# Performance work log

Measured on AMD Instinct MI355X. Metric: run time of the kernel, lower is better.

Reference implementation:

```python
import jax, jax.numpy as jnp
import numpy as np

N_NODES = 100000
N_EDGES = 1600000
N_GRAPHS = 64
FEAT = 64
EMB = 64
HID = 64
VOCAB = 32


def setup_inputs() -> dict:
    key = jax.random.key(0)
    ks = jax.random.split(key, 20)
    w = lambda k, sh: (jax.random.normal(k, sh, jnp.float32) * 0.05)
    x = jax.random.normal(ks[0], (N_NODES, FEAT), jnp.float32)
    edge_index = jax.random.randint(ks[1], (2, N_EDGES), 0, N_NODES, dtype=jnp.int32).astype(jnp.int64)
    batch = jnp.sort(jax.random.randint(ks[2], (N_NODES,), 0, N_GRAPHS, dtype=jnp.int32)).astype(jnp.int64)
    return {
        'x': x, 'edge_index': edge_index, 'batch': batch,
        # RGCN layer 1 (single relation): relation weight, root weight, bias
        'W1': w(ks[3], (FEAT, EMB)), 'root1': w(ks[4], (FEAT, EMB)), 'b1': w(ks[5], (EMB,)),
        # RGCN layer 2
        'W2': w(ks[6], (EMB, HID)), 'root2': w(ks[7], (EMB, HID)), 'b2': w(ks[8], (HID,)),
        # init_h / init_c linear heads
        'Wh': w(ks[9], (HID, HID)), 'bh': w(ks[10], (HID,)),
        'Wc': w(ks[11], (HID, HID)), 'bc': w(ks[12], (HID,)),
        # output layer
        'Wo': w(ks[13], (HID, VOCAB)), 'bo': w(ks[14], (VOCAB,)),
    }


def _rgcn(x, edge_index, W, root, b):
    # PyG RGCNConv with num_relations=1, aggr='mean':
    # out[i] = mean_{j in N(i)} (x[j] @ W) + x[i] @ root + b
    src, dst = edge_index[0], edge_index[1]
    msg = x[src] @ W                                    # [E, out] gather + small GEMM
    agg = jax.ops.segment_sum(msg, dst, num_segments=x.shape[0])
    cnt = jax.ops.segment_sum(jnp.ones((edge_index.shape[1],), x.dtype), dst, num_segments=x.shape[0])
    agg = agg / jnp.maximum(cnt, 1.0)[:, None]
    return agg + x @ root + b


def reference(x, edge_index, batch, W1, root1, b1, W2, root2, b2, Wh, bh, Wc, bc, Wo, bo):
    h = jax.nn.relu(_rgcn(x, edge_index, W1, root1, b1))
    h = jax.nn.relu(_rgcn(h, edge_index, W2, root2, b2))
    # global_mean_pool over graph-assignment vector `batch`
    summ = jax.ops.segment_sum(h, batch, num_segments=N_GRAPHS)
    cnt = jax.ops.segment_sum(jnp.ones((h.shape[0],), h.dtype), batch, num_segments=N_GRAPHS)
    pooled = summ / jnp.maximum(cnt, 1.0)[:, None]      # [G, HID]
    hidden = pooled @ Wh + bh
    cell = pooled @ Wc + bc
    logits = jax.nn.log_softmax(hidden @ Wo + bo, axis=1)
    return (logits, hidden, cell)
```

## Files before the change

### kernel.cpp

```cpp
#include <hip/hip_runtime.h>
#include <hip/hip_bf16.h>


typedef __attribute__((ext_vector_type(8))) short short8;
typedef __attribute__((ext_vector_type(4))) float f32x4;
typedef __attribute__((ext_vector_type(2))) float f32x2;

#define RB 9
#define MAXBINS 256
#define CAP 12288
#define BCAP 14336
#define CHUNK 8192

__device__ inline float bf2f(unsigned short h) {
    return __uint_as_float(((unsigned int)h) << 16);
}
__device__ inline float bflo(unsigned int u) { return __uint_as_float(u << 16); }
__device__ inline float bfhi(unsigned int u) { return __uint_as_float(u & 0xffff0000u); }
__device__ inline unsigned short f2bf(float f) {
    unsigned int u = __float_as_uint(f);
    u = (u + 0x7fffu + ((u >> 16) & 1u)) >> 16;
    return (unsigned short)u;
}

__device__ inline void build_bfrag(const float* __restrict__ W,
                                   const float* __restrict__ R,
                                   int q, int mm, short8 bfrag[8][2]) {
#pragma unroll
    for (int t = 0; t < 8; ++t) {
        const int n = t * 16 + mm;
        const float* P = (n < 64) ? (W + n) : (R + n - 64);
#pragma unroll
        for (int c = 0; c < 2; ++c) {
#pragma unroll
            for (int j = 0; j < 8; ++j) {
                const int k = c * 32 + q * 8 + j;
                bfrag[t][c][j] = (short)f2bf(P[k * 64]);
            }
        }
    }
}

__device__ inline void store_xw_fp8(unsigned char* __restrict__ xw8, int rowbase, int q,
                                    int t, int mm, const f32x4& accT, int N) {
#pragma unroll
    for (int r = 0; r < 4; ++r) {
        const float v0 = accT[r];
        const float v1 = __shfl_down(v0, 1);
        const float v2 = __shfl_down(v0, 2);
        const float v3 = __shfl_down(v0, 3);
        const int orow = rowbase + q * 4 + r;
        if (!(mm & 3) && orow < N) {
            unsigned int u = (unsigned int)__builtin_amdgcn_cvt_pk_fp8_f32(v0, v1, 0, false);
            u = (unsigned int)__builtin_amdgcn_cvt_pk_fp8_f32(v2, v3, (int)u, true);
            *(unsigned int*)&xw8[(size_t)orow * 64 + t * 16 + mm] = u;
        }
    }
}

__global__ __launch_bounds__(256) void bin_gemm1(const int* __restrict__ src,
                                                 const int* __restrict__ dst,
                                                 unsigned int* __restrict__ coarse,
                                                 int* __restrict__ gcur,
                                                 int E, int BINS, int nbBin,
                                                 const float* __restrict__ x,
                                                 const float* __restrict__ W1,
                                                 const float* __restrict__ R1,
                                                 const float* __restrict__ bias,
                                                 unsigned char* __restrict__ xw8,
                                                 unsigned short* __restrict__ xrb,
                                                 int N) {
    __shared__ int cnt[MAXBINS];
    __shared__ int incl[MAXBINS];
    __shared__ int bstart[MAXBINS];
    __shared__ int bcur[MAXBINS];
    __shared__ int gbase[MAXBINS];
    __shared__ unsigned int stage[CHUNK];
    __shared__ unsigned char binOf[CHUNK];

    const int tid = threadIdx.x;
    if (blockIdx.x >= (unsigned)nbBin) {
        const int gb = blockIdx.x - nbBin;
        if (gb == 0 && tid < 16)
            *(unsigned int*)&xw8[(size_t)N * 64 + tid * 4] = 0u;

        const int lane = tid & 63;
        const int q = lane >> 4;
        const int mm = lane & 15;

        short8 bfrag[8][2];
        build_bfrag(W1, R1, q, mm, bfrag);
        float bv[4];
#pragma unroll
        for (int tt = 0; tt < 4; ++tt) bv[tt] = bias[tt * 16 + mm];

        const int wid = tid >> 6;
        const int gw = gb * 4 + wid;
        const int nw = 1024 * 4;
        const int ntiles = N >> 4;

        for (int tile = gw; tile < ntiles; tile += nw) {
            const int row0 = tile << 4;
            const float* ap = &x[(size_t)(row0 + mm) * 64 + q * 8];
            const float4 f0 = *(const float4*)ap;
            const float4 f1 = *(const float4*)(ap + 4);
            const float4 f2 = *(const float4*)(ap + 32);
            const float4 f3 = *(const float4*)(ap + 36);
            short8 a0, a1;
            a0[0] = (short)f2bf(f0.x); a0[1] = (short)f2bf(f0.y);
            a0[2] = (short)f2bf(f0.z); a0[3] = (short)f2bf(f0.w);
            a0[4] = (short)f2bf(f1.x); a0[5] = (short)f2bf(f1.y);
            a0[6] = (short)f2bf(f1.z); a0[7] = (short)f2bf(f1.w);
            a1[0] = (short)f2bf(f2.x); a1[1] = (short)f2bf(f2.y);
            a1[2] = (short)f2bf(f2.z); a1[3] = (short)f2bf(f2.w);
            a1[4] = (short)f2bf(f3.x); a1[5] = (short)f2bf(f3.y);
            a1[6] = (short)f2bf(f3.z); a1[7] = (short)f2bf(f3.w);
            f32x4 acc[8];
#pragma unroll
            for (int t = 0; t < 8; ++t) {
                acc[t] = (f32x4){0.f, 0.f, 0.f, 0.f};
                acc[t] = __builtin_amdgcn_mfma_f32_16x16x32_bf16(a0, bfrag[t][0], acc[t], 0, 0, 0);
                acc[t] = __builtin_amdgcn_mfma_f32_16x16x32_bf16(a1, bfrag[t][1], acc[t], 0, 0, 0);
            }
#pragma unroll
            for (int t = 0; t < 4; ++t) store_xw_fp8(xw8, row0, q, t, mm, acc[t], N);
#pragma unroll
            for (int t = 4; t < 8; ++t) {
#pragma unroll
                for (int r = 0; r < 4; ++r) {
                    const float v = acc[t][r] + bv[t - 4];
                    const float vn = __shfl_down(v, 1);
                    if (!(mm & 1)) {
                        const unsigned int u = (unsigned int)f2bf(v) | ((unsigned int)f2bf(vn) << 16);
                        *(unsigned int*)&xrb[(size_t)(row0 + q * 4 + r) * 64 + (t - 4) * 16 + mm] = u;
                    }
                }
            }
        }
        return;
    }

    const int chunk0 = blockIdx.x * CHUNK;
    int myS[32], myD[32];
#pragma unroll
    for (int k = 0; k < 32; ++k) {
        const int idx = chunk0 + k * 256 + tid;
        if (idx < E) { myS[k] = src[idx]; myD[k] = dst[idx]; }
        else myD[k] = -1;
    }
    cnt[tid] = 0;
    __syncthreads();
#pragma unroll
    for (int k = 0; k < 32; ++k)
        if (myD[k] >= 0) atomicAdd(&cnt[myD[k] >> RB], 1);
    __syncthreads();
    incl[tid] = cnt[tid];
    __syncthreads();
    for (int off = 1; off < 256; off <<= 1) {
        int t = (tid >= off) ? incl[tid - off] : 0;
        __syncthreads();
        incl[tid] += t;
        __syncthreads();
    }
    bstart[tid] = incl[tid] - cnt[tid];
    bcur[tid] = incl[tid] - cnt[tid];
    __syncthreads();
#pragma unroll
    for (int k = 0; k < 32; ++k) {
        if (myD[k] >= 0) {
            const int b = myD[k] >> RB;
            const int pos = atomicAdd(&bcur[b], 1);
            stage[pos] = (unsigned int)myS[k] | ((unsigned int)(myD[k] & ((1 << RB) - 1)) << 17);
            binOf[pos] = (unsigned char)b;
        }
    }
    __syncthreads();
    if (tid < BINS && cnt[tid] > 0)
        gbase[tid] = tid * CAP + atomicAdd(&gcur[tid], cnt[tid]);
    __syncthreads();
    int total = E - chunk0;
    if (total > CHUNK) total = CHUNK;
    for (int idx = tid; idx < total; idx += 256) {
        const int b = binOf[idx];
        coarse[gbase[b] + (idx - bstart[b])] = stage[idx];
    }
}

__global__ __launch_bounds__(256) void finalize_csr(const unsigned int* __restrict__ coarse,
                                                    const int* __restrict__ gcur,
                                                    int* __restrict__ bucket,
                                                    int* __restrict__ pstart,
                                                    int* __restrict__ degarr,
                                                    int N, int BINS) {
    __shared__ int ncnt[512];
    __shared__ int pexcl[512];
    __shared__ int ncur[512];
    __shared__ int s2[256];

    const int tid = threadIdx.x;
    const int b = blockIdx.x;
    const int cb = gcur[b];
    const int base = b * BCAP;
    const unsigned int* reg = coarse + (size_t)b * CAP;
    const int node0 = b << RB;
    int nloc = N - node0;
    if (nloc > 512) nloc = 512;

    ncnt[tid] = 0; ncnt[tid + 256] = 0;
    __syncthreads();
    for (int idx = tid; idx < cb; idx += 256)
        atomicAdd(&ncnt[reg[idx] >> 17], 1);
    __syncthreads();
    const int p0 = (ncnt[2 * tid] + 15) & ~15;
    const int p1 = (ncnt[2 * tid + 1] + 15) & ~15;
    s2[tid] = p0 + p1;
    __syncthreads();
    for (int off = 1; off < 256; off <<= 1) {
        int t = (tid >= off) ? s2[tid - off] : 0;
        __syncthreads();
        s2[tid] += t;
        __syncthreads();
    }
    const int pairExcl = s2[tid] - (p0 + p1);
    pexcl[2 * tid] = pairExcl;
    pexcl[2 * tid + 1] = pairExcl + p0;
    ncur[2 * tid] = pairExcl;
    ncur[2 * tid + 1] = pairExcl + p0;
    __syncthreads();
    for (int i = tid; i < nloc; i += 256) {
        pstart[node0 + i] = base + pexcl[i];
        degarr[node0 + i] = ncnt[i];
        const int dg = ncnt[i];
        const int pd = (dg + 15) & ~15;
        for (int j = dg; j < pd; ++j) bucket[base + pexcl[i] + j] = N;
    }
    for (int idx = tid; idx < cb; idx += 256) {
        const unsigned int e = reg[idx];
        const int p = atomicAdd(&ncur[e >> 17], 1);
        bucket[base + p] = (int)(e & 0x1FFFFu);
    }
}

__global__ __launch_bounds__(256) void aggregate(const unsigned char* __restrict__ xw8,
                                                 const unsigned short* __restrict__ xrb,
                                                 const int* __restrict__ pstart,
                                                 const int* __restrict__ degarr,
                                                 const int* __restrict__ bucket,
                                                 unsigned short* __restrict__ outb,
                                                 int N) {
    const int lane = threadIdx.x & 63;
    const int quarter = lane >> 4;
    const int fl = lane & 15;
    const int wid = threadIdx.x >> 6;
    const int gw = blockIdx.x * 4 + wid;
    const int nw = gridDim.x * 4;

    for (int i = gw; i < N; i += 2 * nw) {
        const int iA = i;
        const int iB = i + nw;
        const bool hasB = iB < N;
        const int r0A = pstart[iA];
        const int dgA = degarr[iA];
        int r0B = r0A, dgB = 0;
        if (hasB) { r0B = pstart[iB]; dgB = degarr[iB]; }
        const int pdA = (dgA + 15) & ~15;
        const int pdB = (dgB + 15) & ~15;
        const int pdM = pdA > pdB ? pdA : pdB;

        float aA0 = 0.f, aA1 = 0.f, aA2 = 0.f, aA3 = 0.f;
        float aB0 = 0.f, aB1 = 0.f, aB2 = 0.f, aB3 = 0.f;
        for (int base = 0; base < pdM; base += 64) {
            const int remA = pdA - base;
            const int remB = pdB - base;
            const int sA = (lane < remA) ? bucket[r0A + base + lane] : N;
            const int sB = (lane < remB) ? bucket[r0B + base + lane] : N;
            int mx = pdM - base;
            if (mx > 64) mx = 64;
            for (int t = 0; t < mx; t += 16) {
                unsigned int uA[4], uB[4];
#pragma unroll
                for (int p = 0; p < 4; ++p) {
                    const int rrA = __shfl(sA, t + 4 * p + quarter);
                    uA[p] = *(const unsigned int*)&xw8[(size_t)rrA * 64 + fl * 4];
                }
#pragma unroll
                for (int p = 0; p < 4; ++p) {
                    const int rrB = __shfl(sB, t + 4 * p + quarter);
                    uB[p] = *(const unsigned int*)&xw8[(size_t)rrB * 64 + fl * 4];
                }
#pragma unroll
                for (int p = 0; p < 4; ++p) {
                    const f32x2 lo = __builtin_amdgcn_cvt_pk_f32_fp8(uA[p], false);
                    const f32x2 hi = __builtin_amdgcn_cvt_pk_f32_fp8(uA[p], true);
                    aA0 += lo.x; aA1 += lo.y; aA2 += hi.x; aA3 += hi.y;
                }
#pragma unroll
                for (int p = 0; p < 4; ++p) {
                    const f32x2 lo = __builtin_amdgcn_cvt_pk_f32_fp8(uB[p], false);
                    const f32x2 hi = __builtin_amdgcn_cvt_pk_f32_fp8(uB[p], true);
                    aB0 += lo.x; aB1 += lo.y; aB2 += hi.x; aB3 += hi.y;
                }
            }
        }
        aA0 += __shfl_xor(aA0, 16); aA1 += __shfl_xor(aA1, 16);
        aA2 += __shfl_xor(aA2, 16); aA3 += __shfl_xor(aA3, 16);
        aA0 += __shfl_xor(aA0, 32); aA1 += __shfl_xor(aA1, 32);
        aA2 += __shfl_xor(aA2, 32); aA3 += __shfl_xor(aA3, 32);
        aB0 += __shfl_xor(aB0, 16); aB1 += __shfl_xor(aB1, 16);
        aB2 += __shfl_xor(aB2, 16); aB3 += __shfl_xor(aB3, 16);
        aB0 += __shfl_xor(aB0, 32); aB1 += __shfl_xor(aB1, 32);
        aB2 += __shfl_xor(aB2, 32); aB3 += __shfl_xor(aB3, 32);

        if (quarter == 0) {
            const float invA = 1.0f / (float)(dgA > 0 ? dgA : 1);
            const uint2 urA = *(const uint2*)&xrb[(size_t)iA * 64 + fl * 4];
            const float o0 = fmaxf(aA0 * invA + bflo(urA.x), 0.f);
            const float o1 = fmaxf(aA1 * invA + bfhi(urA.x), 0.f);
            const float o2 = fmaxf(aA2 * invA + bflo(urA.y), 0.f);
            const float o3 = fmaxf(aA3 * invA + bfhi(urA.y), 0.f);
            uint2 w;
            w.x = (unsigned int)f2bf(o0) | ((unsigned int)f2bf(o1) << 16);
            w.y = (unsigned int)f2bf(o2) | ((unsigned int)f2bf(o3) << 16);
            *(uint2*)&outb[(size_t)iA * 64 + fl * 4] = w;
            if (hasB) {
                const float invB = 1.0f / (float)(dgB > 0 ? dgB : 1);
                const uint2 urB = *(const uint2*)&xrb[(size_t)iB * 64 + fl * 4];
                const float p0 = fmaxf(aB0 * invB + bflo(urB.x), 0.f);
                const float p1 = fmaxf(aB1 * invB + bfhi(urB.x), 0.f);
                const float p2 = fmaxf(aB2 * invB + bflo(urB.y), 0.f);
                const float p3 = fmaxf(aB3 * invB + bfhi(urB.y), 0.f);
                uint2 w2;
                w2.x = (unsigned int)f2bf(p0) | ((unsigned int)f2bf(p1) << 16);
                w2.y = (unsigned int)f2bf(p2) | ((unsigned int)f2bf(p3) << 16);
                *(uint2*)&outb[(size_t)iB * 64 + fl * 4] = w2;
            }
        }
    }
}

__global__ __launch_bounds__(256) void gemm_xwr2(const unsigned short* __restrict__ xin,
                                                 const float* __restrict__ W2,
                                                 const float* __restrict__ R2,
                                                 const float* __restrict__ bias,
                                                 unsigned char* __restrict__ xw8,
                                                 unsigned short* __restrict__ xrb,
                                                 int M) {
    if (blockIdx.x == 0 && threadIdx.x < 16)
        *(unsigned int*)&xw8[(size_t)M * 64 + threadIdx.x * 4] = 0u;

    const int lane = threadIdx.x & 63;
    const int q = lane >> 4;
    const int mm = lane & 15;

    short8 bfrag[8][2];
    build_bfrag(W2, R2, q, mm, bfrag);
    float bv[4];
#pragma unroll
    for (int tt = 0; tt < 4; ++tt) bv[tt] = bias[tt * 16 + mm];

    const int wid = threadIdx.x >> 6;
    const int gw = blockIdx.x * 4 + wid;
    const int nw = gridDim.x * 4;
    const int ntiles = M >> 4;

    for (int tile = gw; tile < ntiles; tile += nw) {
        const int row0 = tile << 4;
        const short8 a0 = *(const short8*)&xin[(size_t)(row0 + mm) * 64 + q * 8];
        const short8 a1 = *(const short8*)&xin[(size_t)(row0 + mm) * 64 + 32 + q * 8];
        f32x4 acc[8];
#pragma unroll
        for (int t = 0; t < 8; ++t) {
            acc[t] = (f32x4){0.f, 0.f, 0.f, 0.f};
            acc[t] = __builtin_amdgcn_mfma_f32_16x16x32_bf16(a0, bfrag[t][0], acc[t], 0, 0, 0);
            acc[t] = __builtin_amdgcn_mfma_f32_16x16x32_bf16(a1, bfrag[t][1], acc[t], 0, 0, 0);
        }
#pragma unroll
        for (int t = 0; t < 4; ++t) store_xw_fp8(xw8, row0, q, t, mm, acc[t], M);
#pragma unroll
        for (int t = 4; t < 8; ++t) {
#pragma unroll
            for (int r = 0; r < 4; ++r) {
                const float v = acc[t][r] + bv[t - 4];
                const float vn = __shfl_down(v, 1);
                if (!(mm & 1)) {
                    const unsigned int u = (unsigned int)f2bf(v) | ((unsigned int)f2bf(vn) << 16);
                    *(unsigned int*)&xrb[(size_t)(row0 + q * 4 + r) * 64 + (t - 4) * 16 + mm] = u;
                }
            }
        }
    }
}

__global__ __launch_bounds__(256) void pool_kernel(const unsigned short* __restrict__ h,
                                                   const int* __restrict__ batch,
                                                   float* __restrict__ pooled, int N) {
    __shared__ float red[16][64];
    __shared__ int bnds[2];
    const int gph = blockIdx.x;
    if (threadIdx.x < 2) {
        const int target = gph + threadIdx.x;
        int lo = 0, hi = N;
        while (lo < hi) {
            int mid = (lo + hi) >> 1;
            if (batch[mid] < target) lo = mid + 1; else hi = mid;
        }
        bnds[threadIdx.x] = lo;
    }
    __syncthreads();
    const int r0 = bnds[0], r1 = bnds[1];
    const int f = threadIdx.x & 15;
    const int r = threadIdx.x >> 4;
    float4 acc = {0.f, 0.f, 0.f, 0.f};
    for (int row = r0 + r; row < r1; row += 16) {
        const ushort4 v = *(const ushort4*)&h[(size_t)row * 64 + f * 4];
        acc.x += bf2f(v.x); acc.y += bf2f(v.y);
        acc.z += bf2f(v.z); acc.w += bf2f(v.w);
    }
    red[r][f * 4 + 0] = acc.x; red[r][f * 4 + 1] = acc.y;
    red[r][f * 4 + 2] = acc.z; red[r][f * 4 + 3] = acc.w;
    __syncthreads();
    if (threadIdx.x < 64) {
        float s = 0.f;
        for (int j = 0; j < 16; ++j) s += red[j][threadIdx.x];
        const int cnt = r1 - r0;
        const float invc = 1.0f / (float)(cnt > 0 ? cnt : 1);
        pooled[gph * 64 + threadIdx.x] = s * invc;
    }
}

__global__ __launch_bounds__(256) void head_kernel(const float* __restrict__ pooled,
                                                   const float* __restrict__ Wh,
                                                   const float* __restrict__ bh,
                                                   const float* __restrict__ Wc,
                                                   const float* __restrict__ bc,
                                                   const float* __restrict__ Wo,
                                                   const float* __restrict__ bo,
                                                   float* __restrict__ out) {
    __shared__ float pm[4096];
    __shared__ float Ws[4096];
    __shared__ float Cs[4096];
    __shared__ float hid[4096];
    const int t = threadIdx.x;

    for (int idx = t; idx < 1024; idx += 256) {
        ((float4*)pm)[idx] = ((const float4*)pooled)[idx];
        ((float4*)Ws)[idx] = ((const float4*)Wh)[idx];
        ((float4*)Cs)[idx] = ((const float4*)Wc)[idx];
    }
    __syncthreads();

    const int w = t >> 6;
    const int l = t & 63;
    const float bhv = bh[l], bcv = bc[l];
    float ah[16], ac[16];
#pragma unroll
    for (int i = 0; i < 16; ++i) { ah[i] = bhv; ac[i] = bcv; }
    const float* pmw = pm + ((w << 4) << 6);
#pragma unroll 4
    for (int k = 0; k < 64; ++k) {
        const float wv = Ws[(k << 6) + l];
        const float cv = Cs[(k << 6) + l];
#pragma unroll
        for (int i = 0; i < 16; ++i) {
            const float p = pmw[(i << 6) + k];
            ah[i] = fmaf(p, wv, ah[i]);
            ac[i] = fmaf(p, cv, ac[i]);
        }
    }
#pragma unroll
    for (int i = 0; i < 16; ++i) {
        const int g = (w << 4) + i;
        hid[(g << 6) + l] = ah[i];
        out[2048 + (g << 6) + l] = ah[i];
        out[6144 + (g << 6) + l] = ac[i];
    }
    __syncthreads();
    for (int idx = t; idx < 512; idx += 256)
        ((float4*)Ws)[idx] = ((const float4*)Wo)[idx];
    __syncthreads();

    const int v = l & 31;
    const int gh = l >> 5;
    const int g0 = ((w << 1) + gh) << 3;
    const float bov = bo[v];
    float lgacc[8];
#pragma unroll
    for (int i = 0; i < 8; ++i) lgacc[i] = bov;
#pragma unroll 4
    for (int k = 0; k < 64; ++k) {
        const float wv = Ws[(k << 5) + v];
#pragma unroll
        for (int i = 0; i < 8; ++i)
            lgacc[i] = fmaf(hid[((g0 + i) << 6) + k], wv, lgacc[i]);
    }
    float* lg = pm;
#pragma unroll
    for (int i = 0; i < 8; ++i) lg[((g0 + i) << 5) + v] = lgacc[i];
    __syncthreads();

    const int g = t >> 2;
    const int vs = (t & 3) << 3;
    const float* row = lg + (g << 5);
    float mx = -3.4e38f;
#pragma unroll
    for (int j = 0; j < 8; ++j) mx = fmaxf(mx, row[vs + j]);
    mx = fmaxf(mx, __shfl_xor(mx, 1));
    mx = fmaxf(mx, __shfl_xor(mx, 2));
    float s = 0.f;
#pragma unroll
    for (int j = 0; j < 8; ++j) s += __expf(row[vs + j] - mx);
    s += __shfl_xor(s, 1);
    s += __shfl_xor(s, 2);
    const float lse = mx + __logf(s);
#pragma unroll
    for (int j = 0; j < 8; ++j) out[(g << 5) + vs + j] = row[vs + j] - lse;
}

extern "C" void kernel_launch(void* const* d_in, const int* in_sizes, int n_in,
                              void* d_out, int out_size, void* d_ws, size_t ws_size,
                              hipStream_t stream) {
    const float* x = (const float*)d_in[0];
    const int* ei = (const int*)d_in[1];
    const int* batch = (const int*)d_in[2];
    const float* W1 = (const float*)d_in[3];
    const float* root1 = (const float*)d_in[4];
    const float* b1 = (const float*)d_in[5];
    const float* W2 = (const float*)d_in[6];
    const float* root2 = (const float*)d_in[7];
    const float* b2 = (const float*)d_in[8];
    const float* Wh = (const float*)d_in[9];
    const float* bh = (const float*)d_in[10];
    const float* Wc = (const float*)d_in[11];
    const float* bc = (const float*)d_in[12];
    const float* Wo = (const float*)d_in[13];
    const float* bo = (const float*)d_in[14];
    float* out = (float*)d_out;

    const int N = in_sizes[0] / 64;
    const int E = in_sizes[1] / 2;
    const int* srcp = ei;
    const int* dstp = ei + E;
    const int BINS = (N + (1 << RB) - 1) >> RB;

    char* ws = (char*)d_ws;
    size_t off = 0;
    auto alloc = [&](size_t bytes) -> void* {
        void* p = ws + off;
        off += (bytes + 255) & ~(size_t)255;
        return p;
    };
    int* pstart = (int*)alloc((size_t)N * 4);
    int* degarr = (int*)alloc((size_t)N * 4);
    int* bucket = (int*)alloc(((size_t)BINS * BCAP + 256) * 4);
    unsigned int* coarse = (unsigned int*)alloc((size_t)BINS * CAP * 4);
    unsigned short* h1 = (unsigned short*)alloc((size_t)N * 64 * 2);
    unsigned short* h2 = (unsigned short*)alloc((size_t)N * 64 * 2);
    unsigned char* xw8 = (unsigned char*)alloc((size_t)(N + 1) * 64);
    unsigned char* xw8b = (unsigned char*)alloc((size_t)(N + 1) * 64);
    unsigned short* xrb = (unsigned short*)alloc((size_t)N * 64 * 2);
    unsigned short* xrb2 = (unsigned short*)alloc((size_t)N * 64 * 2);
    float* pooled = (float*)alloc(4096 * 4);
    int* gcur = (int*)alloc(MAXBINS * 4);

    const int nbBin = (E + CHUNK - 1) / CHUNK;

    hipMemsetAsync(gcur, 0, MAXBINS * 4, stream);
    bin_gemm1<<<nbBin + 1024, 256, 0, stream>>>(srcp, dstp, coarse, gcur, E, BINS, nbBin,
                                                x, W1, root1, b1, xw8, xrb, N);
    finalize_csr<<<BINS, 256, 0, stream>>>(coarse, gcur, bucket, pstart, degarr, N, BINS);
    aggregate<<<4096, 256, 0, stream>>>(xw8, xrb, pstart, degarr, bucket, h1, N);
    gemm_xwr2<<<1024, 256, 0, stream>>>(h1, W2, root2, b2, xw8b, xrb2, N);
    aggregate<<<4096, 256, 0, stream>>>(xw8b, xrb2, pstart, degarr, bucket, h2, N);
    pool_kernel<<<64, 256, 0, stream>>>(h2, batch, pooled, N);
    head_kernel<<<1, 256, 0, stream>>>(pooled, Wh, bh, Wc, bc, Wo, bo, out);
}
```

Baseline: 263.8 us.

## Split pooling across four blocks per graph and skip padded gather work in aggregate

```diff
diff --git a/kernel.cpp b/kernel.cpp
--- a/kernel.cpp
+++ b/kernel.cpp
@@ -254,6 +254,7 @@
     const int wid = threadIdx.x >> 6;
     const int gw = blockIdx.x * 4 + wid;
     const int nw = gridDim.x * 4;
+    const unsigned flo = (unsigned)(fl << 2);
 
     for (int i = gw; i < N; i += 2 * nw) {
         const int iA = i;
@@ -272,33 +273,48 @@
         for (int base = 0; base < pdM; base += 64) {
             const int remA = pdA - base;
             const int remB = pdB - base;
-            const int sA = (lane < remA) ? bucket[r0A + base + lane] : N;
-            const int sB = (lane < remB) ? bucket[r0B + base + lane] : N;
+            int sA = N, sB = N;
+            if (remA > 0 && lane < remA)
+                sA = *(const int*)((const char*)bucket + ((unsigned)(r0A + base + lane) << 2));
+            if (remB > 0 && lane < remB)
+                sB = *(const int*)((const char*)bucket + ((unsigned)(r0B + base + lane) << 2));
+            const int mxA = remA < 64 ? remA : 64;
+            const int mxB = remB < 64 ? remB : 64;
             int mx = pdM - base;
             if (mx > 64) mx = 64;
             for (int t = 0; t < mx; t += 16) {
+                const bool doA = t < mxA;
+                const bool doB = t < mxB;
                 unsigned int uA[4], uB[4];
-#pragma unroll
-                for (int p = 0; p < 4; ++p) {
-                    const int rrA = __shfl(sA, t + 4 * p + quarter);
-                    uA[p] = *(const unsigned int*)&xw8[(size_t)rrA * 64 + fl * 4];
+                if (doA) {
+#pragma unroll
+                    for (int p = 0; p < 4; ++p) {
+                        const unsigned rr = (unsigned)__shfl(sA, t + 4 * p + quarter);
+                        uA[p] = *(const unsigned int*)(xw8 + ((rr << 6) | flo));
+                    }
                 }
-#pragma unroll
-                for (int p = 0; p < 4; ++p) {
-                    const int rrB = __shfl(sB, t + 4 * p + quarter);
-                    uB[p] = *(const unsigned int*)&xw8[(size_t)rrB * 64 + fl * 4];
+                if (doB) {
+#pragma unroll
+                    for (int p = 0; p < 4; ++p) {
+                        const unsigned rr = (unsigned)__shfl(sB, t + 4 * p + quarter);
+                        uB[p] = *(const unsigned int*)(xw8 + ((rr << 6) | flo));
+                    }
                 }
-#pragma unroll
-                for (int p = 0; p < 4; ++p) {
-                    const f32x2 lo = __builtin_amdgcn_cvt_pk_f32_fp8(uA[p], false);
-                    const f32x2 hi = __builtin_amdgcn_cvt_pk_f32_fp8(uA[p], true);
-                    aA0 += lo.x; aA1 += lo.y; aA2 += hi.x; aA3 += hi.y;
+                if (doA) {
+#pragma unroll
+                    for (int p = 0; p < 4; ++p) {
+                        const f32x2 lo = __builtin_amdgcn_cvt_pk_f32_fp8(uA[p], false);
+                        const f32x2 hi = __builtin_amdgcn_cvt_pk_f32_fp8(uA[p], true);
+                        aA0 += lo.x; aA1 += lo.y; aA2 += hi.x; aA3 += hi.y;
+                    }
                 }
-#pragma unroll
-                for (int p = 0; p < 4; ++p) {
-                    const f32x2 lo = __builtin_amdgcn_cvt_pk_f32_fp8(uB[p], false);
-                    const f32x2 hi = __builtin_amdgcn_cvt_pk_f32_fp8(uB[p], true);
-                    aB0 += lo.x; aB1 += lo.y; aB2 += hi.x; aB3 += hi.y;
+                if (doB) {
+#pragma unroll
+                    for (int p = 0; p < 4; ++p) {
+                        const f32x2 lo = __builtin_amdgcn_cvt_pk_f32_fp8(uB[p], false);
+                        const f32x2 hi = __builtin_amdgcn_cvt_pk_f32_fp8(uB[p], true);
+                        aB0 += lo.x; aB1 += lo.y; aB2 += hi.x; aB3 += hi.y;
+                    }
                 }
             }
         }
@@ -393,10 +409,11 @@
 
 __global__ __launch_bounds__(256) void pool_kernel(const unsigned short* __restrict__ h,
                                                    const int* __restrict__ batch,
-                                                   float* __restrict__ pooled, int N) {
+                                                   float* __restrict__ gsum, int N) {
     __shared__ float red[16][64];
     __shared__ int bnds[2];
-    const int gph = blockIdx.x;
+    const int gph = blockIdx.x >> 2;
+    const int part = blockIdx.x & 3;
     if (threadIdx.x < 2) {
         const int target = gph + threadIdx.x;
         int lo = 0, hi = N;
@@ -407,11 +424,13 @@
         bnds[threadIdx.x] = lo;
     }
     __syncthreads();
-    const int r0 = bnds[0], r1 = bnds[1];
+    const int r0 = bnds[0], tot = bnds[1] - bnds[0];
+    const int pr0 = r0 + (tot * part) / 4;
+    const int pr1 = r0 + (tot * (part + 1)) / 4;
     const int f = threadIdx.x & 15;
     const int r = threadIdx.x >> 4;
     float4 acc = {0.f, 0.f, 0.f, 0.f};
-    for (int row = r0 + r; row < r1; row += 16) {
+    for (int row = pr0 + r; row < pr1; row += 16) {
         const ushort4 v = *(const ushort4*)&h[(size_t)row * 64 + f * 4];
         acc.x += bf2f(v.x); acc.y += bf2f(v.y);
         acc.z += bf2f(v.z); acc.w += bf2f(v.w);
@@ -422,28 +441,42 @@
     if (threadIdx.x < 64) {
         float s = 0.f;
         for (int j = 0; j < 16; ++j) s += red[j][threadIdx.x];
-        const int cnt = r1 - r0;
-        const float invc = 1.0f / (float)(cnt > 0 ? cnt : 1);
-        pooled[gph * 64 + threadIdx.x] = s * invc;
-    }
-}
-
-__global__ __launch_bounds__(256) void head_kernel(const float* __restrict__ pooled,
+        atomicAdd(&gsum[gph * 64 + threadIdx.x], s);
+    }
+}
+
+__global__ __launch_bounds__(256) void head_kernel(const float* __restrict__ gsum,
+                                                   const int* __restrict__ batch,
                                                    const float* __restrict__ Wh,
                                                    const float* __restrict__ bh,
                                                    const float* __restrict__ Wc,
                                                    const float* __restrict__ bc,
                                                    const float* __restrict__ Wo,
                                                    const float* __restrict__ bo,
-                                                   float* __restrict__ out) {
+                                                   float* __restrict__ out, int N) {
     __shared__ float pm[4096];
     __shared__ float Ws[4096];
     __shared__ float Cs[4096];
     __shared__ float hid[4096];
+    __shared__ int bnds[65];
     const int t = threadIdx.x;
 
+    if (t < 65) {
+        int lo = 0, hi = N;
+        while (lo < hi) {
+            int mid = (lo + hi) >> 1;
+            if (batch[mid] < t) lo = mid + 1; else hi = mid;
+        }
+        bnds[t] = lo;
+    }
+    __syncthreads();
     for (int idx = t; idx < 1024; idx += 256) {
-        ((float4*)pm)[idx] = ((const float4*)pooled)[idx];
+        const int g = idx >> 4;
+        const int c = bnds[g + 1] - bnds[g];
+        const float inv = 1.0f / (float)(c > 0 ? c : 1);
+        float4 v = ((const float4*)gsum)[idx];
+        v.x *= inv; v.y *= inv; v.z *= inv; v.w *= inv;
+        ((float4*)pm)[idx] = v;
         ((float4*)Ws)[idx] = ((const float4*)Wh)[idx];
         ((float4*)Cs)[idx] = ((const float4*)Wc)[idx];
     }
@@ -559,18 +592,18 @@
     unsigned char* xw8b = (unsigned char*)alloc((size_t)(N + 1) * 64);
     unsigned short* xrb = (unsigned short*)alloc((size_t)N * 64 * 2);
     unsigned short* xrb2 = (unsigned short*)alloc((size_t)N * 64 * 2);
-    float* pooled = (float*)alloc(4096 * 4);
     int* gcur = (int*)alloc(MAXBINS * 4);
+    float* gsum = (float*)alloc(4096 * 4);
 
     const int nbBin = (E + CHUNK - 1) / CHUNK;
 
-    hipMemsetAsync(gcur, 0, MAXBINS * 4, stream);
+    hipMemsetAsync(gcur, 0, MAXBINS * 4 + 4096 * 4, stream);
     bin_gemm1<<<nbBin + 1024, 256, 0, stream>>>(srcp, dstp, coarse, gcur, E, BINS, nbBin,
                                                 x, W1, root1, b1, xw8, xrb, N);
     finalize_csr<<<BINS, 256, 0, stream>>>(coarse, gcur, bucket, pstart, degarr, N, BINS);
     aggregate<<<4096, 256, 0, stream>>>(xw8, xrb, pstart, degarr, bucket, h1, N);
     gemm_xwr2<<<1024, 256, 0, stream>>>(h1, W2, root2, b2, xw8b, xrb2, N);
     aggregate<<<4096, 256, 0, stream>>>(xw8b, xrb2, pstart, degarr, bucket, h2, N);
-    pool_kernel<<<64, 256, 0, stream>>>(h2, batch, pooled, N);
-    head_kernel<<<1, 256, 0, stream>>>(pooled, Wh, bh, Wc, bc, Wo, bo, out);
-}
+    pool_kernel<<<256, 256, 0, stream>>>(h2, batch, gsum, N);
+    head_kernel<<<1, 256, 0, stream>>>(gsum, batch, Wh, bh, Wc, bc, Wo, bo, out, N);
+}
```

Measured after the change: 246.5 us. -6.5%, faster.
